# Kernel optimization log

Measured on AMD Instinct MI355X. Metric: run time of the kernel, lower is better.

## Reference

```python
import jax, jax.numpy as jnp
import numpy as np

# pywt db4 decomposition filters (8 taps)
DEC_LO = np.array([-0.010597401784997278, 0.032883011666982945, 0.030841381835986965,
                   -0.18703481171888114, -0.02798376941698385, 0.6308807679295904,
                   0.7148465705525415, 0.23037781330885523], dtype=np.float32)
DEC_HI = np.array([-0.23037781330885523, 0.7148465705525415, -0.6308807679295904,
                   -0.02798376941698385, 0.18703481171888114, 0.030841381835986965,
                   -0.032883011666982945, -0.010597401784997278], dtype=np.float32)
LEVEL = 6
F = 8  # filter length

# pywt dwt with mode='zero' is exactly full_convolve(x, filt)[1::2].
# We realize it as a strided correlation with the flipped filters:
# out[i] = sum_j x_pad[2i+j] * filt[F-1-j], x padded left by F-2 zeros.
_KERNEL = jnp.asarray(np.stack([DEC_LO[::-1], DEC_HI[::-1]])[:, None, :])  # [2,1,F]

def _dwt_step(x):
    # x: [B, N] -> (cA [B, M], cD [B, M]) with M = floor((N+F-1)/2)
    N = x.shape[-1]
    M = (N + F - 1) // 2
    xp = jnp.pad(x, ((0, 0), (F - 2, F)))[:, None, :]          # [B,1,Npad]
    y = jax.lax.conv_general_dilated(
        xp, _KERNEL.astype(x.dtype), window_strides=(2,), padding='VALID',
        dimension_numbers=('NCH', 'OIH', 'NCH'))                # [B,2,>=M]
    return y[:, 0, :M], y[:, 1, :M]


def setup_inputs() -> dict:
    key = jax.random.key(0)
    x = jax.random.normal(key, (64, 262144), dtype=jnp.float32)
    return {"x": x}


def reference(x):
    # Cascaded 6-level db4 DWT, zero boundary mode.
    a = x
    details = []  # finest first
    for _ in range(LEVEL):
        a, d = _dwt_step(a)
        details.append(d)
    # Match torch module: details[0] = coarsest detail (pywt coeffs[1])
    return (a,) + tuple(details[::-1])
```

## Files before the change

kernel.cpp:

```cpp
#include <hip/hip_runtime.h>


#define NT 256
#define TT 64
#define LEN0 4474
#define LEN1 2234
#define LEN2 1114
#define LEN3 554
#define LEN4 274
#define LEN5 134

#define N0 262144
#define M1 131075
#define M2 65541
#define M3 32774
#define M4 16390
#define M5 8198
#define M6 4102

#define OFF_A6 ((size_t)0)
#define OFF_D6 ((size_t)262528)
#define OFF_D5 ((size_t)525056)
#define OFF_D4 ((size_t)1049728)
#define OFF_D3 ((size_t)2098688)
#define OFF_D2 ((size_t)4196224)
#define OFF_D1 ((size_t)8390848)

__device__ __constant__ float RLO[8] = {
    0.23037781330885523f, 0.7148465705525415f, 0.6308807679295904f,
    -0.02798376941698385f, -0.18703481171888114f, 0.030841381835986965f,
    0.032883011666982945f, -0.010597401784997278f};
__device__ __constant__ float RHI[8] = {
    -0.010597401784997278f, -0.032883011666982945f, 0.030841381835986965f,
    0.18703481171888114f, -0.02798376941698385f, -0.6308807679295904f,
    0.7148465705525415f, -0.23037781330885523f};

template <int LEN, int NC>
__device__ __forceinline__ void level_fast(const float4* __restrict__ s4,
                                           float4* __restrict__ d4,
                                           float* __restrict__ dg) {
  for (int c = threadIdx.x; c < NC; c += NT) {
    float4 q0 = s4[2 * c + 0];
    float4 q1 = s4[2 * c + 1];
    float4 q2 = s4[2 * c + 2];
    float4 q3 = s4[2 * c + 3];
    float w[16] = {q0.x, q0.y, q0.z, q0.w, q1.x, q1.y, q1.z, q1.w,
                   q2.x, q2.y, q2.z, q2.w, q3.x, q3.y, q3.z, q3.w};
    float a[4], d[4];
#pragma unroll
    for (int j = 0; j < 4; ++j) {
      float aa = 0.f, dd = 0.f;
#pragma unroll
      for (int m = 0; m < 8; ++m) {
        aa = fmaf(RLO[m], w[2 * j + m], aa);
        dd = fmaf(RHI[m], w[2 * j + m], dd);
      }
      a[j] = aa;
      d[j] = dd;
    }
    d4[c] = make_float4(a[0], a[1], a[2], a[3]);
    const int l0 = 4 * c;
    if (l0 + 4 <= LEN) {
#pragma unroll
      for (int j = 0; j < 4; ++j) dg[l0 + j] = d[j];
    } else {
#pragma unroll
      for (int j = 0; j < 4; ++j)
        if (l0 + j < LEN) dg[l0 + j] = d[j];
    }
  }
}

__device__ inline void dwt_step_slow(const float* __restrict__ s,
                                     float* __restrict__ d, int base, int len,
                                     int M, int cOff, float* __restrict__ dglob,
                                     int tid) {
  for (int l = tid; l < len; l += NT) {
    int g = base + l;
    float a = 0.f, dt = 0.f;
    if (g >= 0 && g < M) {
#pragma unroll
      for (int m = 0; m < 8; ++m) {
        float v = s[2 * l + m];
        a = fmaf(RLO[m], v, a);
        dt = fmaf(RHI[m], v, dt);
      }
    }
    d[l] = a;
    if (l >= cOff && g < M) dglob[g] = dt;
  }
}

__global__ __launch_bounds__(NT, 5) void dwt6_kernel(const float* __restrict__ x,
                                                     float* __restrict__ out) {
  const int p = blockIdx.x;
  const int row = blockIdx.y;
  const int tid = threadIdx.x;

  __shared__ float4 bufA4[1120];
  __shared__ float4 bufB4[560];
  float* bufA = (float*)bufA4;
  float* bufB = (float*)bufB4;

  const int b6 = p * TT;
  const int b5 = 2 * b6 - 6;
  const int b4 = 2 * b5 - 6;
  const int b3 = 2 * b4 - 6;
  const int b2 = 2 * b3 - 6;
  const int b1 = 2 * b2 - 6;
  const int b0 = 2 * b1 - 6;

  const size_t r1 = (size_t)row * M1, r2 = (size_t)row * M2,
               r3 = (size_t)row * M3, r4 = (size_t)row * M4,
               r5 = (size_t)row * M5, r6 = (size_t)row * M6;

  if (p >= 1 && p <= 63) {
    const float2* __restrict__ xs = (const float2*)(x + (size_t)row * N0 + b0);
    float2* __restrict__ bA2 = (float2*)bufA;
    for (int m = tid; m < LEN0 / 2; m += NT) bA2[m] = xs[m];
    __syncthreads();

    level_fast<LEN1, 559>(bufA4, bufB4, out + OFF_D1 + r1 + b1);
    __syncthreads();
    level_fast<LEN2, 279>(bufB4, bufA4, out + OFF_D2 + r2 + b2);
    __syncthreads();
    level_fast<LEN3, 139>(bufA4, bufB4, out + OFF_D3 + r3 + b3);
    __syncthreads();
    level_fast<LEN4, 69>(bufB4, bufA4, out + OFF_D4 + r4 + b4);
    __syncthreads();
    level_fast<LEN5, 34>(bufA4, bufB4, out + OFF_D5 + r5 + b5);
    __syncthreads();

    float* __restrict__ ga = out + OFF_A6 + r6 + b6;
    float* __restrict__ gd = out + OFF_D6 + r6 + b6;
    for (int c = tid; c < 16; c += NT) {
      float4 q0 = bufB4[2 * c + 0];
      float4 q1 = bufB4[2 * c + 1];
      float4 q2 = bufB4[2 * c + 2];
      float4 q3 = bufB4[2 * c + 3];
      float w[16] = {q0.x, q0.y, q0.z, q0.w, q1.x, q1.y, q1.z, q1.w,
                     q2.x, q2.y, q2.z, q2.w, q3.x, q3.y, q3.z, q3.w};
#pragma unroll
      for (int j = 0; j < 4; ++j) {
        float aa = 0.f, dd = 0.f;
#pragma unroll
        for (int m = 0; m < 8; ++m) {
          aa = fmaf(RLO[m], w[2 * j + m], aa);
          dd = fmaf(RHI[m], w[2 * j + m], dd);
        }
        ga[4 * c + j] = aa;
        gd[4 * c + j] = dd;
      }
    }
  } else {
    const float* __restrict__ xr = x + (size_t)row * N0;
    for (int l = tid; l < LEN0; l += NT) {
      int g = b0 + l;
      bufA[l] = (g >= 0 && g < N0) ? xr[g] : 0.0f;
    }
    __syncthreads();

    dwt_step_slow(bufA, bufB, b1, LEN1, M1, 186, out + OFF_D1 + r1, tid);
    __syncthreads();
    dwt_step_slow(bufB, bufA, b2, LEN2, M2, 90, out + OFF_D2 + r2, tid);
    __syncthreads();
    dwt_step_slow(bufA, bufB, b3, LEN3, M3, 42, out + OFF_D3 + r3, tid);
    __syncthreads();
    dwt_step_slow(bufB, bufA, b4, LEN4, M4, 18, out + OFF_D4 + r4, tid);
    __syncthreads();
    dwt_step_slow(bufA, bufB, b5, LEN5, M5, 6, out + OFF_D5 + r5, tid);
    __syncthreads();

    for (int l = tid; l < TT; l += NT) {
      int g = b6 + l;
      if (g < M6) {
        float a = 0.f, dt = 0.f;
#pragma unroll
        for (int m = 0; m < 8; ++m) {
          float v = bufB[2 * l + m];
          a = fmaf(RLO[m], v, a);
          dt = fmaf(RHI[m], v, dt);
        }
        out[OFF_A6 + r6 + g] = a;
        out[OFF_D6 + r6 + g] = dt;
      }
    }
  }
}

extern "C" void kernel_launch(void* const* d_in, const int* in_sizes, int n_in,
                              void* d_out, int out_size, void* d_ws,
                              size_t ws_size, hipStream_t stream) {
  const float* x = (const float*)d_in[0];
  float* out = (float*)d_out;
  dim3 grid(65, 64);
  dwt6_kernel<<<grid, NT, 0, stream>>>(x, out);
}
```

Before: 123.7 us.

## Halve tile size, use even/odd-split LDS layout, nontemporal stores

Halves the per-block output tile, doubles the grid and raises launch bounds to 8 blocks per CU. Shared-memory buffers are now split into even and odd planes, so each level reads contiguous float4s and writes its approximation output as float2 pairs into the next level's planes. Global input is loaded as float4 and de-interleaved on the fly, and detail stores become nontemporal. The aim is higher occupancy, fewer bank conflicts and less cache pollution, at the cost of more halo recomputation from overlap in the smaller tiles.

```diff
diff --git a/kernel.cpp b/kernel.cpp
--- a/kernel.cpp
+++ b/kernel.cpp
@@ -2,13 +2,13 @@
 
 
 #define NT 256
-#define TT 64
-#define LEN0 4474
-#define LEN1 2234
-#define LEN2 1114
-#define LEN3 554
-#define LEN4 274
-#define LEN5 134
+#define TT 32
+#define LEN0 2426
+#define LEN1 1210
+#define LEN2 602
+#define LEN3 298
+#define LEN4 146
+#define LEN5 70
 
 #define N0 262144
 #define M1 131075
@@ -25,6 +25,12 @@
 #define OFF_D3 ((size_t)2098688)
 #define OFF_D2 ((size_t)4196224)
 #define OFF_D1 ((size_t)8390848)
+
+#define AE 0
+#define AO 1216
+#define BE 2432
+#define BO 3040
+#define LDS_FLOATS 3648
 
 __device__ __constant__ float RLO[8] = {
     0.23037781330885523f, 0.7148465705525415f, 0.6308807679295904f,
@@ -35,38 +41,43 @@
     0.18703481171888114f, -0.02798376941698385f, -0.6308807679295904f,
     0.7148465705525415f, -0.23037781330885523f};
 
-template <int LEN, int NC>
-__device__ __forceinline__ void level_fast(const float4* __restrict__ s4,
-                                           float4* __restrict__ d4,
+template <int LEN, int NC, int SHIFT>
+__device__ __forceinline__ void level_fast(const float4* __restrict__ sE4,
+                                           const float4* __restrict__ sO4,
+                                           float2* __restrict__ dE2,
+                                           float2* __restrict__ dO2,
                                            float* __restrict__ dg) {
   for (int c = threadIdx.x; c < NC; c += NT) {
-    float4 q0 = s4[2 * c + 0];
-    float4 q1 = s4[2 * c + 1];
-    float4 q2 = s4[2 * c + 2];
-    float4 q3 = s4[2 * c + 3];
-    float w[16] = {q0.x, q0.y, q0.z, q0.w, q1.x, q1.y, q1.z, q1.w,
-                   q2.x, q2.y, q2.z, q2.w, q3.x, q3.y, q3.z, q3.w};
+    float4 e0 = sE4[c], e1 = sE4[c + 1];
+    float4 o0 = sO4[c], o1 = sO4[c + 1];
+    float e[8] = {e0.x, e0.y, e0.z, e0.w, e1.x, e1.y, e1.z, e1.w};
+    float o[8] = {o0.x, o0.y, o0.z, o0.w, o1.x, o1.y, o1.z, o1.w};
     float a[4], d[4];
 #pragma unroll
     for (int j = 0; j < 4; ++j) {
       float aa = 0.f, dd = 0.f;
 #pragma unroll
-      for (int m = 0; m < 8; ++m) {
-        aa = fmaf(RLO[m], w[2 * j + m], aa);
-        dd = fmaf(RHI[m], w[2 * j + m], dd);
+      for (int t = 0; t < 4; ++t) {
+        float ev = e[j + t + SHIFT];
+        float ov = o[j + t + SHIFT];
+        aa = fmaf(RLO[2 * t], ev, aa);
+        aa = fmaf(RLO[2 * t + 1], ov, aa);
+        dd = fmaf(RHI[2 * t], ev, dd);
+        dd = fmaf(RHI[2 * t + 1], ov, dd);
       }
       a[j] = aa;
       d[j] = dd;
     }
-    d4[c] = make_float4(a[0], a[1], a[2], a[3]);
+    dE2[c] = make_float2(a[0], a[2]);
+    dO2[c] = make_float2(a[1], a[3]);
     const int l0 = 4 * c;
     if (l0 + 4 <= LEN) {
 #pragma unroll
-      for (int j = 0; j < 4; ++j) dg[l0 + j] = d[j];
+      for (int j = 0; j < 4; ++j) __builtin_nontemporal_store(d[j], dg + l0 + j);
     } else {
 #pragma unroll
       for (int j = 0; j < 4; ++j)
-        if (l0 + j < LEN) dg[l0 + j] = d[j];
+        if (l0 + j < LEN) __builtin_nontemporal_store(d[j], dg + l0 + j);
     }
   }
 }
@@ -91,16 +102,13 @@
   }
 }
 
-__global__ __launch_bounds__(NT, 5) void dwt6_kernel(const float* __restrict__ x,
+__global__ __launch_bounds__(NT, 8) void dwt6_kernel(const float* __restrict__ x,
                                                      float* __restrict__ out) {
   const int p = blockIdx.x;
   const int row = blockIdx.y;
   const int tid = threadIdx.x;
 
-  __shared__ float4 bufA4[1120];
-  __shared__ float4 bufB4[560];
-  float* bufA = (float*)bufA4;
-  float* bufB = (float*)bufB4;
+  __shared__ float lds[LDS_FLOATS];
 
   const int b6 = p * TT;
   const int b5 = 2 * b6 - 6;
@@ -114,45 +122,60 @@
                r3 = (size_t)row * M3, r4 = (size_t)row * M4,
                r5 = (size_t)row * M5, r6 = (size_t)row * M6;
 
-  if (p >= 1 && p <= 63) {
-    const float2* __restrict__ xs = (const float2*)(x + (size_t)row * N0 + b0);
-    float2* __restrict__ bA2 = (float2*)bufA;
-    for (int m = tid; m < LEN0 / 2; m += NT) bA2[m] = xs[m];
-    __syncthreads();
-
-    level_fast<LEN1, 559>(bufA4, bufB4, out + OFF_D1 + r1 + b1);
-    __syncthreads();
-    level_fast<LEN2, 279>(bufB4, bufA4, out + OFF_D2 + r2 + b2);
-    __syncthreads();
-    level_fast<LEN3, 139>(bufA4, bufB4, out + OFF_D3 + r3 + b3);
-    __syncthreads();
-    level_fast<LEN4, 69>(bufB4, bufA4, out + OFF_D4 + r4 + b4);
-    __syncthreads();
-    level_fast<LEN5, 34>(bufA4, bufB4, out + OFF_D5 + r5 + b5);
+  if (p >= 1 && p <= 127) {
+    const float4* __restrict__ xs4 =
+        (const float4*)(x + (size_t)row * N0 + (b0 - 2));
+    float2* __restrict__ aE2 = (float2*)(lds + AE);
+    float2* __restrict__ aO2 = (float2*)(lds + AO);
+    for (int m = tid; m < 607; m += NT) {
+      float4 v = xs4[m];
+      aE2[m] = make_float2(v.x, v.z);
+      aO2[m] = make_float2(v.y, v.w);
+    }
+    __syncthreads();
+
+    const float4* aE4 = (const float4*)(lds + AE);
+    const float4* aO4 = (const float4*)(lds + AO);
+    const float4* bE4 = (const float4*)(lds + BE);
+    const float4* bO4 = (const float4*)(lds + BO);
+    float2* bE2 = (float2*)(lds + BE);
+    float2* bO2 = (float2*)(lds + BO);
+
+    level_fast<LEN1, 303, 1>(aE4, aO4, bE2, bO2, out + OFF_D1 + r1 + b1);
+    __syncthreads();
+    level_fast<LEN2, 151, 0>(bE4, bO4, aE2, aO2, out + OFF_D2 + r2 + b2);
+    __syncthreads();
+    level_fast<LEN3, 75, 0>(aE4, aO4, bE2, bO2, out + OFF_D3 + r3 + b3);
+    __syncthreads();
+    level_fast<LEN4, 37, 0>(bE4, bO4, aE2, aO2, out + OFF_D4 + r4 + b4);
+    __syncthreads();
+    level_fast<LEN5, 18, 0>(aE4, aO4, bE2, bO2, out + OFF_D5 + r5 + b5);
     __syncthreads();
 
     float* __restrict__ ga = out + OFF_A6 + r6 + b6;
     float* __restrict__ gd = out + OFF_D6 + r6 + b6;
-    for (int c = tid; c < 16; c += NT) {
-      float4 q0 = bufB4[2 * c + 0];
-      float4 q1 = bufB4[2 * c + 1];
-      float4 q2 = bufB4[2 * c + 2];
-      float4 q3 = bufB4[2 * c + 3];
-      float w[16] = {q0.x, q0.y, q0.z, q0.w, q1.x, q1.y, q1.z, q1.w,
-                     q2.x, q2.y, q2.z, q2.w, q3.x, q3.y, q3.z, q3.w};
+    for (int c = tid; c < 8; c += NT) {
+      float4 e0 = bE4[c], e1 = bE4[c + 1];
+      float4 o0 = bO4[c], o1 = bO4[c + 1];
+      float e[8] = {e0.x, e0.y, e0.z, e0.w, e1.x, e1.y, e1.z, e1.w};
+      float o[8] = {o0.x, o0.y, o0.z, o0.w, o1.x, o1.y, o1.z, o1.w};
 #pragma unroll
       for (int j = 0; j < 4; ++j) {
         float aa = 0.f, dd = 0.f;
 #pragma unroll
-        for (int m = 0; m < 8; ++m) {
-          aa = fmaf(RLO[m], w[2 * j + m], aa);
-          dd = fmaf(RHI[m], w[2 * j + m], dd);
+        for (int t = 0; t < 4; ++t) {
+          aa = fmaf(RLO[2 * t], e[j + t], aa);
+          aa = fmaf(RLO[2 * t + 1], o[j + t], aa);
+          dd = fmaf(RHI[2 * t], e[j + t], dd);
+          dd = fmaf(RHI[2 * t + 1], o[j + t], dd);
         }
-        ga[4 * c + j] = aa;
-        gd[4 * c + j] = dd;
+        __builtin_nontemporal_store(aa, ga + 4 * c + j);
+        __builtin_nontemporal_store(dd, gd + 4 * c + j);
       }
     }
   } else {
+    float* bufA = lds;
+    float* bufB = lds + BE;
     const float* __restrict__ xr = x + (size_t)row * N0;
     for (int l = tid; l < LEN0; l += NT) {
       int g = b0 + l;
@@ -193,6 +216,6 @@
                               size_t ws_size, hipStream_t stream) {
   const float* x = (const float*)d_in[0];
   float* out = (float*)d_out;
-  dim3 grid(65, 64);
+  dim3 grid(129, 64);
   dwt6_kernel<<<grid, NT, 0, stream>>>(x, out);
 }
```

After: 113.9 us. 1.09x faster.

## Split DWT cascade into two kernels with workspace and even/odd LDS layout

Applied to the files above, without the earlier changes.

The single six-level fused kernel becomes two kernels. The first computes levels 1-2 from the input with smaller tiles and writes the level-2 approximation to a workspace. The second reads that workspace and computes levels 3-6. This cuts the large halo recomputation and LDS footprint of the deep fused tile, which allows higher occupancy. It also stores LDS data de-interleaved into even and odd lanes for vector reads and uses nontemporal global stores for the detail outputs. In exchange it adds a second launch and a round trip of the level-2 approximation through global memory.

```diff
diff --git a/kernel.cpp b/kernel.cpp
--- a/kernel.cpp
+++ b/kernel.cpp
@@ -2,13 +2,6 @@
 
 
 #define NT 256
-#define TT 64
-#define LEN0 4474
-#define LEN1 2234
-#define LEN2 1114
-#define LEN3 554
-#define LEN4 274
-#define LEN5 134
 
 #define N0 262144
 #define M1 131075
@@ -17,6 +10,7 @@
 #define M4 16390
 #define M5 8198
 #define M6 4102
+#define WSTRIDE 65544
 
 #define OFF_A6 ((size_t)0)
 #define OFF_D6 ((size_t)262528)
@@ -25,6 +19,9 @@
 #define OFF_D3 ((size_t)2098688)
 #define OFF_D2 ((size_t)4196224)
 #define OFF_D1 ((size_t)8390848)
+
+typedef float f4_t __attribute__((ext_vector_type(4)));
+typedef f4_t f4u_t __attribute__((aligned(4)));
 
 __device__ __constant__ float RLO[8] = {
     0.23037781330885523f, 0.7148465705525415f, 0.6308807679295904f,
@@ -35,154 +32,243 @@
     0.18703481171888114f, -0.02798376941698385f, -0.6308807679295904f,
     0.7148465705525415f, -0.23037781330885523f};
 
-template <int LEN, int NC>
-__device__ __forceinline__ void level_fast(const float4* __restrict__ s4,
-                                           float4* __restrict__ d4,
-                                           float* __restrict__ dg) {
+template <int NC, int SLO, int SHI, int SHIFT, bool A_GLOBAL, bool A_NT>
+__device__ __forceinline__ void level_fast(const f4_t* __restrict__ sE4,
+                                           const f4_t* __restrict__ sO4,
+                                           float2* __restrict__ dE2,
+                                           float2* __restrict__ dO2,
+                                           float* __restrict__ gA,
+                                           float* __restrict__ gD) {
   for (int c = threadIdx.x; c < NC; c += NT) {
-    float4 q0 = s4[2 * c + 0];
-    float4 q1 = s4[2 * c + 1];
-    float4 q2 = s4[2 * c + 2];
-    float4 q3 = s4[2 * c + 3];
-    float w[16] = {q0.x, q0.y, q0.z, q0.w, q1.x, q1.y, q1.z, q1.w,
-                   q2.x, q2.y, q2.z, q2.w, q3.x, q3.y, q3.z, q3.w};
+    f4_t e0 = sE4[c], e1 = sE4[c + 1];
+    f4_t o0 = sO4[c], o1 = sO4[c + 1];
+    float e[8] = {e0.x, e0.y, e0.z, e0.w, e1.x, e1.y, e1.z, e1.w};
+    float o[8] = {o0.x, o0.y, o0.z, o0.w, o1.x, o1.y, o1.z, o1.w};
     float a[4], d[4];
 #pragma unroll
     for (int j = 0; j < 4; ++j) {
       float aa = 0.f, dd = 0.f;
 #pragma unroll
-      for (int m = 0; m < 8; ++m) {
-        aa = fmaf(RLO[m], w[2 * j + m], aa);
-        dd = fmaf(RHI[m], w[2 * j + m], dd);
+      for (int t = 0; t < 4; ++t) {
+        float ev = e[j + t + SHIFT], ov = o[j + t + SHIFT];
+        aa = fmaf(RLO[2 * t], ev, aa);
+        aa = fmaf(RLO[2 * t + 1], ov, aa);
+        dd = fmaf(RHI[2 * t], ev, dd);
+        dd = fmaf(RHI[2 * t + 1], ov, dd);
       }
       a[j] = aa;
       d[j] = dd;
     }
-    d4[c] = make_float4(a[0], a[1], a[2], a[3]);
+    if (A_GLOBAL) {
+      f4_t av = {a[0], a[1], a[2], a[3]};
+      if (A_NT)
+        __builtin_nontemporal_store(av, (f4u_t*)(gA + 4 * c));
+      else
+        *(f4u_t*)(gA + 4 * c) = av;
+    } else {
+      dE2[c] = make_float2(a[0], a[2]);
+      dO2[c] = make_float2(a[1], a[3]);
+    }
     const int l0 = 4 * c;
-    if (l0 + 4 <= LEN) {
-#pragma unroll
-      for (int j = 0; j < 4; ++j) dg[l0 + j] = d[j];
+    const int lo = l0 < SLO ? SLO : l0;
+    const int hi = (l0 + 4) < SHI ? (l0 + 4) : SHI;
+    if (lo == l0 && hi == l0 + 4) {
+      f4_t dv = {d[0], d[1], d[2], d[3]};
+      __builtin_nontemporal_store(dv, (f4u_t*)(gD + l0));
     } else {
-#pragma unroll
-      for (int j = 0; j < 4; ++j)
-        if (l0 + j < LEN) dg[l0 + j] = d[j];
+      for (int j = lo - l0; j < hi - l0; ++j)
+        __builtin_nontemporal_store(d[j], gD + l0 + j);
     }
   }
 }
 
-__device__ inline void dwt_step_slow(const float* __restrict__ s,
-                                     float* __restrict__ d, int base, int len,
-                                     int M, int cOff, float* __restrict__ dglob,
-                                     int tid) {
-  for (int l = tid; l < len; l += NT) {
-    int g = base + l;
-    float a = 0.f, dt = 0.f;
-    if (g >= 0 && g < M) {
-#pragma unroll
-      for (int m = 0; m < 8; ++m) {
-        float v = s[2 * l + m];
-        a = fmaf(RLO[m], v, a);
-        dt = fmaf(RHI[m], v, dt);
-      }
-    }
-    d[l] = a;
-    if (l >= cOff && g < M) dglob[g] = dt;
+__global__ __launch_bounds__(NT, 8) void dwt_k1(const float* __restrict__ x,
+                                                float* __restrict__ out,
+                                                float* __restrict__ ws) {
+  const int q = blockIdx.x;
+  const int row = blockIdx.y;
+  const int tid = threadIdx.x;
+  __shared__ float lds[3112];
+
+  const int b2 = q << 9;
+  const int b1h = (q << 10) - 6;
+  const int b0h = (q << 11) - 18;
+
+  float* gD1 = out + OFF_D1 + (size_t)row * M1 + b1h;
+  float* gD2 = out + OFF_D2 + (size_t)row * M2 + b2;
+  float* gA2 = ws + (size_t)row * WSTRIDE + b2;
+
+  if (q >= 1 && q <= 127) {
+    const f4_t* __restrict__ xs4 =
+        (const f4_t*)(x + (size_t)row * N0 + (b0h - 2));
+    float2* Ep2 = (float2*)(lds + 0);
+    float2* Op2 = (float2*)(lds + 1036);
+    for (int m = tid; m < 517; m += NT) {
+      f4_t v = xs4[m];
+      Ep2[m] = make_float2(v.x, v.z);
+      Op2[m] = make_float2(v.y, v.w);
+    }
+    __syncthreads();
+    level_fast<258, 6, 1030, 1, false, false>(
+        (const f4_t*)(lds + 0), (const f4_t*)(lds + 1036),
+        (float2*)(lds + 2072), (float2*)(lds + 2592), nullptr, gD1);
+    __syncthreads();
+    level_fast<128, 0, 512, 0, true, false>(
+        (const f4_t*)(lds + 2072), (const f4_t*)(lds + 2592), nullptr, nullptr,
+        gA2, gD2);
+  } else {
+    float* xf = lds;
+    float* a1 = lds + 2072;
+    const float* __restrict__ xr = x + (size_t)row * N0;
+    for (int l = tid; l < 2072; l += NT) {
+      int g = b0h + l;
+      xf[l] = (g >= 0 && g < N0) ? xr[g] : 0.f;
+    }
+    __syncthreads();
+    const int own0 = q << 10;
+    for (int lA = tid; lA < 1032; lA += NT) {
+      int g = b1h + lA;
+      float aa = 0.f, dd = 0.f;
+      if (g >= 0 && g < M1) {
+#pragma unroll
+        for (int m = 0; m < 8; ++m) {
+          float v = xf[2 * lA + m];
+          aa = fmaf(RLO[m], v, aa);
+          dd = fmaf(RHI[m], v, dd);
+        }
+      }
+      a1[lA] = aa;
+      if (g >= own0 && g < own0 + 1024 && g < M1)
+        __builtin_nontemporal_store(dd, gD1 + lA);
+    }
+    __syncthreads();
+    for (int l = tid; l < 512; l += NT) {
+      int g2 = b2 + l;
+      if (g2 < M2) {
+        float aa = 0.f, dd = 0.f;
+#pragma unroll
+        for (int m = 0; m < 8; ++m) {
+          float v = a1[2 * l + m];
+          aa = fmaf(RLO[m], v, aa);
+          dd = fmaf(RHI[m], v, dd);
+        }
+        __builtin_nontemporal_store(dd, gD2 + l);
+        gA2[l] = aa;
+      }
+    }
   }
 }
 
-__global__ __launch_bounds__(NT, 5) void dwt6_kernel(const float* __restrict__ x,
-                                                     float* __restrict__ out) {
+__global__ __launch_bounds__(NT, 8) void dwt_k2(const float* __restrict__ ws,
+                                                float* __restrict__ out) {
   const int p = blockIdx.x;
   const int row = blockIdx.y;
   const int tid = threadIdx.x;
-
-  __shared__ float4 bufA4[1120];
-  __shared__ float4 bufB4[560];
-  float* bufA = (float*)bufA4;
-  float* bufB = (float*)bufB4;
-
-  const int b6 = p * TT;
-  const int b5 = 2 * b6 - 6;
-  const int b4 = 2 * b5 - 6;
-  const int b3 = 2 * b4 - 6;
-  const int b2 = 2 * b3 - 6;
-  const int b1 = 2 * b2 - 6;
-  const int b0 = 2 * b1 - 6;
-
-  const size_t r1 = (size_t)row * M1, r2 = (size_t)row * M2,
-               r3 = (size_t)row * M3, r4 = (size_t)row * M4,
-               r5 = (size_t)row * M5, r6 = (size_t)row * M6;
+  __shared__ float lds[1680];
+
+  const int b6 = p << 6;
+  const int b5 = (p << 7) - 6;
+  const int b4 = (p << 8) - 18;
+  const int b3 = (p << 9) - 42;
+  const int b2t = (p << 10) - 90;
+
+  float* gD3 = out + OFF_D3 + (size_t)row * M3 + b3;
+  float* gD4 = out + OFF_D4 + (size_t)row * M4 + b4;
+  float* gD5 = out + OFF_D5 + (size_t)row * M5 + b5;
+  float* gD6 = out + OFF_D6 + (size_t)row * M6 + b6;
+  float* gA6 = out + OFF_A6 + (size_t)row * M6 + b6;
+  const float* __restrict__ wr = ws + (size_t)row * WSTRIDE;
 
   if (p >= 1 && p <= 63) {
-    const float2* __restrict__ xs = (const float2*)(x + (size_t)row * N0 + b0);
-    float2* __restrict__ bA2 = (float2*)bufA;
-    for (int m = tid; m < LEN0 / 2; m += NT) bA2[m] = xs[m];
-    __syncthreads();
-
-    level_fast<LEN1, 559>(bufA4, bufB4, out + OFF_D1 + r1 + b1);
-    __syncthreads();
-    level_fast<LEN2, 279>(bufB4, bufA4, out + OFF_D2 + r2 + b2);
-    __syncthreads();
-    level_fast<LEN3, 139>(bufA4, bufB4, out + OFF_D3 + r3 + b3);
-    __syncthreads();
-    level_fast<LEN4, 69>(bufB4, bufA4, out + OFF_D4 + r4 + b4);
-    __syncthreads();
-    level_fast<LEN5, 34>(bufA4, bufB4, out + OFF_D5 + r5 + b5);
-    __syncthreads();
-
-    float* __restrict__ ga = out + OFF_A6 + r6 + b6;
-    float* __restrict__ gd = out + OFF_D6 + r6 + b6;
-    for (int c = tid; c < 16; c += NT) {
-      float4 q0 = bufB4[2 * c + 0];
-      float4 q1 = bufB4[2 * c + 1];
-      float4 q2 = bufB4[2 * c + 2];
-      float4 q3 = bufB4[2 * c + 3];
-      float w[16] = {q0.x, q0.y, q0.z, q0.w, q1.x, q1.y, q1.z, q1.w,
-                     q2.x, q2.y, q2.z, q2.w, q3.x, q3.y, q3.z, q3.w};
-#pragma unroll
-      for (int j = 0; j < 4; ++j) {
-        float aa = 0.f, dd = 0.f;
-#pragma unroll
-        for (int m = 0; m < 8; ++m) {
-          aa = fmaf(RLO[m], w[2 * j + m], aa);
-          dd = fmaf(RHI[m], w[2 * j + m], dd);
-        }
-        ga[4 * c + j] = aa;
-        gd[4 * c + j] = dd;
-      }
-    }
+    const f4_t* __restrict__ s4 = (const f4_t*)(wr + (b2t - 2));
+    float2* Ep2 = (float2*)(lds + 0);
+    float2* Op2 = (float2*)(lds + 560);
+    for (int m = tid; m < 279; m += NT) {
+      f4_t v = s4[m];
+      Ep2[m] = make_float2(v.x, v.z);
+      Op2[m] = make_float2(v.y, v.w);
+    }
+    __syncthreads();
+    level_fast<139, 0, 554, 1, false, false>(
+        (const f4_t*)(lds + 0), (const f4_t*)(lds + 560),
+        (float2*)(lds + 1120), (float2*)(lds + 1400), nullptr, gD3);
+    __syncthreads();
+    level_fast<69, 0, 274, 0, false, false>(
+        (const f4_t*)(lds + 1120), (const f4_t*)(lds + 1400),
+        (float2*)(lds + 0), (float2*)(lds + 560), nullptr, gD4);
+    __syncthreads();
+    level_fast<34, 0, 134, 0, false, false>(
+        (const f4_t*)(lds + 0), (const f4_t*)(lds + 560),
+        (float2*)(lds + 1120), (float2*)(lds + 1400), nullptr, gD5);
+    __syncthreads();
+    level_fast<16, 0, 64, 0, true, true>(
+        (const f4_t*)(lds + 1120), (const f4_t*)(lds + 1400), nullptr, nullptr,
+        gA6, gD6);
   } else {
-    const float* __restrict__ xr = x + (size_t)row * N0;
-    for (int l = tid; l < LEN0; l += NT) {
-      int g = b0 + l;
-      bufA[l] = (g >= 0 && g < N0) ? xr[g] : 0.0f;
-    }
-    __syncthreads();
-
-    dwt_step_slow(bufA, bufB, b1, LEN1, M1, 186, out + OFF_D1 + r1, tid);
-    __syncthreads();
-    dwt_step_slow(bufB, bufA, b2, LEN2, M2, 90, out + OFF_D2 + r2, tid);
-    __syncthreads();
-    dwt_step_slow(bufA, bufB, b3, LEN3, M3, 42, out + OFF_D3 + r3, tid);
-    __syncthreads();
-    dwt_step_slow(bufB, bufA, b4, LEN4, M4, 18, out + OFF_D4 + r4, tid);
-    __syncthreads();
-    dwt_step_slow(bufA, bufB, b5, LEN5, M5, 6, out + OFF_D5 + r5, tid);
-    __syncthreads();
-
-    for (int l = tid; l < TT; l += NT) {
+    float* xf = lds;
+    float* bb = lds + 1120;
+    for (int l = tid; l < 1116; l += NT) {
+      int g = b2t + l;
+      xf[l] = (g >= 0 && g < M2) ? wr[g] : 0.f;
+    }
+    __syncthreads();
+    for (int l = tid; l < 554; l += NT) {
+      int g = b3 + l;
+      float aa = 0.f, dd = 0.f;
+      if (g >= 0 && g < M3) {
+#pragma unroll
+        for (int m = 0; m < 8; ++m) {
+          float v = xf[2 * l + m];
+          aa = fmaf(RLO[m], v, aa);
+          dd = fmaf(RHI[m], v, dd);
+        }
+      }
+      bb[l] = aa;
+      if (l >= 42 && g < M3) __builtin_nontemporal_store(dd, gD3 + l);
+    }
+    __syncthreads();
+    for (int l = tid; l < 274; l += NT) {
+      int g = b4 + l;
+      float aa = 0.f, dd = 0.f;
+      if (g >= 0 && g < M4) {
+#pragma unroll
+        for (int m = 0; m < 8; ++m) {
+          float v = bb[2 * l + m];
+          aa = fmaf(RLO[m], v, aa);
+          dd = fmaf(RHI[m], v, dd);
+        }
+      }
+      lds[l] = aa;
+      if (l >= 18 && g < M4) __builtin_nontemporal_store(dd, gD4 + l);
+    }
+    __syncthreads();
+    for (int l = tid; l < 134; l += NT) {
+      int g = b5 + l;
+      float aa = 0.f, dd = 0.f;
+      if (g >= 0 && g < M5) {
+#pragma unroll
+        for (int m = 0; m < 8; ++m) {
+          float v = lds[2 * l + m];
+          aa = fmaf(RLO[m], v, aa);
+          dd = fmaf(RHI[m], v, dd);
+        }
+      }
+      bb[l] = aa;
+      if (l >= 6 && g < M5) __builtin_nontemporal_store(dd, gD5 + l);
+    }
+    __syncthreads();
+    for (int l = tid; l < 64; l += NT) {
       int g = b6 + l;
       if (g < M6) {
-        float a = 0.f, dt = 0.f;
-#pragma unroll
-        for (int m = 0; m < 8; ++m) {
-          float v = bufB[2 * l + m];
-          a = fmaf(RLO[m], v, a);
-          dt = fmaf(RHI[m], v, dt);
-        }
-        out[OFF_A6 + r6 + g] = a;
-        out[OFF_D6 + r6 + g] = dt;
+        float aa = 0.f, dd = 0.f;
+#pragma unroll
+        for (int m = 0; m < 8; ++m) {
+          float v = bb[2 * l + m];
+          aa = fmaf(RLO[m], v, aa);
+          dd = fmaf(RHI[m], v, dd);
+        }
+        __builtin_nontemporal_store(aa, gA6 + l);
+        __builtin_nontemporal_store(dd, gD6 + l);
       }
     }
   }
@@ -193,6 +279,7 @@
                               size_t ws_size, hipStream_t stream) {
   const float* x = (const float*)d_in[0];
   float* out = (float*)d_out;
-  dim3 grid(65, 64);
-  dwt6_kernel<<<grid, NT, 0, stream>>>(x, out);
-}
+  float* ws = (float*)d_ws;
+  dwt_k1<<<dim3(129, 64), NT, 0, stream>>>(x, out, ws);
+  dwt_k2<<<dim3(65, 64), NT, 0, stream>>>(ws, out);
+}
```

New measurement: 123.2 us. Within noise of the previous version (-0.4%).
